# Optimization experiments

Hardware: AMD Instinct MI355X
Metric: run time of the kernel (lower is better)

The kernel has to match this reference:

```python
import jax, jax.numpy as jnp
import numpy as np

D_MODEL = 1024
N_HEADS = 16
HEAD_DIM = D_MODEL // N_HEADS
D_LATENT = 256
LAMBDA_DECAY = 0.01
TIME_STEP = 0.01  # get_timestamps spacing; wall-clock base cancels in diffs
CLAMP = 1e4


def setup_inputs() -> dict:
    key = jax.random.key(0)
    ks = jax.random.split(key, 8)
    B, S = 2, 2048
    def w(k, i, o):
        return jax.random.normal(k, (i, o), dtype=jnp.float32) * 0.02
    return {
        "x": jax.random.normal(ks[0], (B, S, D_MODEL), dtype=jnp.float32),
        "Wq": w(ks[1], D_MODEL, D_MODEL),
        "Wk": w(ks[2], D_MODEL, D_MODEL),
        "Wv": w(ks[3], D_MODEL, D_MODEL),
        "Wo": w(ks[4], D_MODEL, D_MODEL),
        "W_down_kv": w(ks[5], D_MODEL, D_LATENT),
        "W_up_k": w(ks[6], D_LATENT, D_MODEL),
        "W_up_v": w(ks[7], D_LATENT, D_MODEL),
    }


def reference(x, Wq, Wk, Wv, Wo, W_down_kv, W_up_k, W_up_v):
    B, S, _ = x.shape
    q = x @ Wq
    k = x @ Wk
    v = x @ Wv
    latent_kv = (k + v) @ W_down_kv            # [B,S,d_latent]
    k_rec = latent_kv @ W_up_k                 # [B,S,d_model]
    v_rec = latent_kv @ W_up_v
    # split heads -> [B,H,S,hd]
    def heads(t):
        return t.reshape(B, S, N_HEADS, HEAD_DIM).transpose(0, 2, 1, 3)
    qh, kh, vh = heads(q), heads(k_rec), heads(v_rec)
    scale = 1.0 / (jnp.sqrt(jnp.float32(D_MODEL)) + 1e-8)
    scores = jnp.einsum("bhqd,bhkd->bhqk", qh, kh) * scale
    scores = jnp.clip(jnp.nan_to_num(scores, nan=-1e9), -CLAMP, CLAMP)
    # time decay: |t_i - t_j| = TIME_STEP * |i - j| (wall-clock base cancels)
    idx = jnp.arange(S, dtype=jnp.float32)
    decay = jnp.exp(-LAMBDA_DECAY * TIME_STEP * jnp.abs(idx[:, None] - idx[None, :]))
    scores = scores * decay[None, None, :, :]
    scores = jnp.clip(jnp.nan_to_num(scores, nan=-1e9), -CLAMP, CLAMP)
    attn = jax.nn.softmax(scores, axis=-1)
    out = jnp.einsum("bhqk,bhkd->bhqd", attn, vh)
    out = out.transpose(0, 2, 1, 3).reshape(B, S, D_MODEL)
    return out @ Wo, latent_kv
```

## Files before the change

kernel.cpp:

```cpp
#include <hip/hip_runtime.h>
#include <hip/hip_bf16.h>
#include <cstdint>
#include <cstddef>

typedef __bf16 bf16;
typedef __bf16 bf16x8 __attribute__((ext_vector_type(8)));
typedef float f32x4 __attribute__((ext_vector_type(4)));

#define NB 2
#define SEQ 2048
#define DM 1024
#define MTOK 4096
#define DL 256
#define NH 16
#define HD 64

#define LOG2E 1.4426950408889634f

__device__ __forceinline__ void gload16(const void* g, void* l) {
  __builtin_amdgcn_global_load_lds((const __attribute__((address_space(1))) void*)g,
                                   (__attribute__((address_space(3))) void*)l, 16, 0, 0);
}
__device__ __forceinline__ float fast_exp2(float x) {
#if __has_builtin(__builtin_amdgcn_exp2f)
  return __builtin_amdgcn_exp2f(x);
#else
  float r; asm("v_exp_f32 %0, %1" : "=v"(r) : "v"(x)); return r;
#endif
}
__device__ __forceinline__ int xcd_swz(int orig, int nwg) {
  int x = orig & 7;
  int q = nwg >> 3, r = nwg & 7;
  int base = (x < r) ? x * (q + 1) : r * (q + 1) + (x - r) * q;
  return base + (orig >> 3);
}

__device__ __forceinline__ void transpose_dev(const float* __restrict__ in0,
                                              bf16* __restrict__ out, int R, int C,
                                              int c0, int r0, int tid, float (*tile)[33]) {
  int tx = tid & 31, ty = tid >> 5;
#pragma unroll
  for (int i = 0; i < 4; ++i) {
    int r = r0 + ty + 8 * i;
    tile[ty + 8 * i][tx] = in0[(size_t)r * C + c0 + tx];
  }
  __syncthreads();
  int c = tid >> 3, s = tid & 7;
  bf16 o4[4] __attribute__((aligned(8)));
#pragma unroll
  for (int j = 0; j < 4; ++j) o4[j] = (bf16)tile[4 * s + j][c];
  *reinterpret_cast<uint2*>(out + (size_t)(c0 + c) * R + r0 + 4 * s) =
      *reinterpret_cast<const uint2*>(o4);
}

__device__ __forceinline__ void cvt8_dev(const float* __restrict__ in, bf16* __restrict__ out,
                                         int blk, int tid) {
  int i = (blk * 256 + tid) * 8;
  float4 a = *reinterpret_cast<const float4*>(in + i);
  float4 b = *reinterpret_cast<const float4*>(in + i + 4);
  bf16 o[8] __attribute__((aligned(16)));
  o[0] = (bf16)a.x; o[1] = (bf16)a.y; o[2] = (bf16)a.z; o[3] = (bf16)a.w;
  o[4] = (bf16)b.x; o[5] = (bf16)b.y; o[6] = (bf16)b.z; o[7] = (bf16)b.w;
  *reinterpret_cast<uint4*>(out + i) = *reinterpret_cast<const uint4*>(o);
}

__device__ __forceinline__ void sum8_dev(const float* __restrict__ in0, const float* __restrict__ in1,
                                         bf16* __restrict__ out, int blk, int tid) {
  int i = (blk * 256 + tid) * 8;
  float4 a0 = *reinterpret_cast<const float4*>(in0 + i);
  float4 b0 = *reinterpret_cast<const float4*>(in0 + i + 4);
  float4 a1 = *reinterpret_cast<const float4*>(in1 + i);
  float4 b1 = *reinterpret_cast<const float4*>(in1 + i + 4);
  bf16 o[8] __attribute__((aligned(16)));
  o[0] = (bf16)(a0.x + a1.x); o[1] = (bf16)(a0.y + a1.y);
  o[2] = (bf16)(a0.z + a1.z); o[3] = (bf16)(a0.w + a1.w);
  o[4] = (bf16)(b0.x + b1.x); o[5] = (bf16)(b0.y + b1.y);
  o[6] = (bf16)(b0.z + b1.z); o[7] = (bf16)(b0.w + b1.w);
  *reinterpret_cast<uint4*>(out + i) = *reinterpret_cast<const uint4*>(o);
}

__global__ __launch_bounds__(256) void prep_kernel(const float* __restrict__ x,
                                                   const float* __restrict__ Wq,
                                                   const float* __restrict__ Wk,
                                                   const float* __restrict__ Wv,
                                                   const float* __restrict__ Wo,
                                                   const float* __restrict__ Wdn,
                                                   const float* __restrict__ Wuk,
                                                   const float* __restrict__ Wuv,
                                                   bf16* xbf, bf16* WqT, bf16* WoT, bf16* WdnT,
                                                   bf16* WukT, bf16* WuvT, bf16* Wkv) {
  __shared__ float tile[32][33];
  int id = blockIdx.x, tid = threadIdx.x;
  if (id < 2048) { cvt8_dev(x, xbf, id, tid); return; }
  id -= 2048;
  if (id < 512) { sum8_dev(Wk, Wv, Wkv, id, tid); return; }
  id -= 512;
  if (id < 1024) { transpose_dev(Wq, WqT, 1024, 1024, (id & 31) * 32, (id >> 5) * 32, tid, tile); return; }
  id -= 1024;
  if (id < 1024) { transpose_dev(Wo, WoT, 1024, 1024, (id & 31) * 32, (id >> 5) * 32, tid, tile); return; }
  id -= 1024;
  if (id < 256) { transpose_dev(Wdn, WdnT, 1024, 256, (id & 7) * 32, (id >> 3) * 32, tid, tile); return; }
  id -= 256;
  if (id < 256) { transpose_dev(Wuk, WukT, 256, 1024, (id & 31) * 32, (id >> 5) * 32, tid, tile); return; }
  id -= 256;
  transpose_dev(Wuv, WuvT, 256, 1024, (id & 31) * 32, (id >> 5) * 32, tid, tile);
}

template <int TN, int EPI>
__device__ __forceinline__ void gemm_core(const bf16* __restrict__ A, const bf16* __restrict__ Bt,
                                          bf16* __restrict__ O1, bf16* __restrict__ O2,
                                          float* __restrict__ Of,
                                          int K, int bx, int by, bf16* As, bf16* Bs) {
  const int tid = threadIdx.x;
  const int lane = tid & 63;
  const int wv = tid >> 6;
  const int wr = wv >> 1, wc = wv & 1;
  const int row0 = bx * 128, col0 = by * TN;
  const int l15 = lane & 15;
  const int kq = (lane >> 4) * 8;
  constexpr int NR = TN / 32;
  constexpr int BSZ = TN * 32;

  const bf16* aS = A + (size_t)(row0 + (tid >> 2)) * K + (tid & 3) * 8;
  const bf16* bS = Bt + (size_t)(col0 + (tid >> 2)) * K + (tid & 3) * 8;
  const int d0 = tid * 8, d1 = tid * 8 + 2048;

  gload16(aS, As + d0); gload16(aS + (size_t)64 * K, As + d1);
  gload16(bS, Bs + d0);
  if constexpr (TN == 128) gload16(bS + (size_t)64 * K, Bs + d1);
  aS += 32; bS += 32;

  f32x4 acc[4][NR] = {};
  int cur = 0;
  for (int k0 = 0; k0 < K; k0 += 32) {
    __syncthreads();
    if (k0 + 32 < K) {
      const int nxA = (cur ^ 1) * 4096, nxB = (cur ^ 1) * BSZ;
      gload16(aS, As + nxA + d0); gload16(aS + (size_t)64 * K, As + nxA + d1);
      gload16(bS, Bs + nxB + d0);
      if constexpr (TN == 128) gload16(bS + (size_t)64 * K, Bs + nxB + d1);
      aS += 32; bS += 32;
    }
    const bf16* Ab = As + cur * 4096;
    const bf16* Bb = Bs + cur * BSZ;
    bf16x8 af[4], bfr[NR];
#pragma unroll
    for (int m = 0; m < 4; ++m)
      af[m] = *reinterpret_cast<const bf16x8*>(&Ab[(wr * 64 + m * 16 + l15) * 32 + kq]);
#pragma unroll
    for (int n = 0; n < NR; ++n)
      bfr[n] = *reinterpret_cast<const bf16x8*>(&Bb[(wc * (TN / 2) + n * 16 + l15) * 32 + kq]);
    __builtin_amdgcn_s_setprio(1);
#pragma unroll
    for (int m = 0; m < 4; ++m)
#pragma unroll
      for (int n = 0; n < NR; ++n)
        acc[m][n] = __builtin_amdgcn_mfma_f32_16x16x32_bf16(af[m], bfr[n], acc[m][n], 0, 0, 0);
    __builtin_amdgcn_s_setprio(0);
    cur ^= 1;
  }

  const int rbase = row0 + wr * 64 + (lane >> 4) * 4;
  const int cbase = col0 + wc * (TN / 2) + l15;
#pragma unroll
  for (int m = 0; m < 4; ++m) {
#pragma unroll
    for (int n = 0; n < NR; ++n) {
      const int cc = cbase + n * 16;
      if constexpr (EPI == 0) {
#pragma unroll
        for (int r = 0; r < 4; ++r)
          O1[(size_t)(rbase + m * 16 + r) * DM + cc] = (bf16)acc[m][n][r];
      } else if constexpr (EPI == 3) {
#pragma unroll
        for (int r = 0; r < 4; ++r)
          Of[(size_t)(rbase + m * 16 + r) * DM + cc] = acc[m][n][r];
      } else if constexpr (EPI == 6) {
#pragma unroll
        for (int r = 0; r < 4; ++r) {
          float v = acc[m][n][r];
          O1[(size_t)(rbase + m * 16 + r) * DL + cc] = (bf16)v;
          Of[(size_t)(rbase + m * 16 + r) * DL + cc] = v;
        }
      } else {
#pragma unroll
        for (int r = 0; r < 4; ++r)
          O1[(size_t)(rbase + m * 16 + r) * MTOK + cc] = (bf16)acc[m][n][r];
      }
    }
  }
}

__global__ __launch_bounds__(256) void gemm_q_w(const bf16* __restrict__ xbf,
                                                const bf16* __restrict__ WqT, bf16* qbf,
                                                const bf16* __restrict__ WdnT,
                                                const bf16* __restrict__ Wkv, bf16* WkvdT) {
  __shared__ __align__(16) bf16 As[2 * 4096];
  __shared__ __align__(16) bf16 Bs[2 * 64 * 32];
  int id = xcd_swz(blockIdx.x, 544);
  if (id < 32)
    gemm_core<64, 0>(WdnT, Wkv, WkvdT, nullptr, nullptr, DM, id >> 4, id & 15, As, Bs);
  else {
    int j = id - 32;
    gemm_core<64, 0>(xbf, WqT, qbf, nullptr, nullptr, DM, j >> 4, j & 15, As, Bs);
  }
}

__global__ __launch_bounds__(256) void gemm_latent(const bf16* __restrict__ xbf,
                                                   const bf16* __restrict__ WkvdT,
                                                   bf16* latbf, float* out_lat) {
  __shared__ __align__(16) bf16 As[2 * 4096];
  __shared__ __align__(16) bf16 Bs[2 * 64 * 32];
  int id = xcd_swz(blockIdx.x, 128);
  gemm_core<64, 6>(xbf, WkvdT, latbf, nullptr, out_lat, DM, id >> 2, id & 3, As, Bs);
}

__global__ __launch_bounds__(256) void gemm_up(const bf16* __restrict__ latbf,
                                               const bf16* __restrict__ WukT,
                                               const bf16* __restrict__ WuvT,
                                               bf16* kbuf, bf16* vT) {
  __shared__ __align__(16) bf16 As[2 * 4096];
  __shared__ __align__(16) bf16 Bs[2 * 64 * 32];
  int id = xcd_swz(blockIdx.x, 1024);
  if (id < 512)
    gemm_core<64, 0>(latbf, WukT, kbuf, nullptr, nullptr, DL, id >> 4, id & 15, As, Bs);
  else {
    int j = id - 512;
    gemm_core<64, 7>(WuvT, latbf, vT, nullptr, nullptr, DL, j >> 6, j & 63, As, Bs);
  }
}

__global__ __launch_bounds__(256) void gemm_out(const bf16* __restrict__ ctx,
                                                const bf16* __restrict__ WoT, float* out0) {
  __shared__ __align__(16) bf16 As[2 * 4096];
  __shared__ __align__(16) bf16 Bs[2 * 64 * 32];
  int id = xcd_swz(blockIdx.x, 512);
  gemm_core<64, 3>(ctx, WoT, nullptr, nullptr, out0, DM, id >> 4, id & 15, As, Bs);
}

__global__ __launch_bounds__(256) void attn_kernel(const bf16* __restrict__ Q,
                                                   const bf16* __restrict__ Kr,
                                                   const bf16* __restrict__ Vt,
                                                   bf16* __restrict__ Ctx) {
  __shared__ __align__(16) bf16 Ks[2 * 4096];
  __shared__ __align__(16) bf16 Vs[2 * 4096];
  __shared__ __align__(16) bf16 Ps[4096];
  const int work = xcd_swz(blockIdx.x, SEQ / 64 * NH * NB);
  const int qt = work & 31, h = (work >> 5) & 15, b = work >> 9;
  const int tid = threadIdx.x, lane = tid & 63, wv = tid >> 6;
  const int l15 = lane & 15, lg = lane >> 4;
  const int qbase = qt * 64 + wv * 16;
  const size_t tok0 = (size_t)b * SEQ;

  bf16x8 qf[2];
  {
    const bf16* qp = Q + (tok0 + qbase + l15) * DM + h * HD + lg * 8;
    qf[0] = *reinterpret_cast<const bf16x8*>(qp);
    qf[1] = *reinterpret_cast<const bf16x8*>(qp + 32);
  }

  const int c1 = tid + 256;
  const int r0s = tid >> 3, r1s = c1 >> 3;
  const int cc0 = (tid & 7) ^ (r0s & 7), cc1 = (c1 & 7) ^ (r1s & 7);
  const bf16* kS0 = Kr + (tok0 + r0s) * DM + h * HD + cc0 * 8;
  const bf16* kS1 = Kr + (tok0 + r1s) * DM + h * HD + cc1 * 8;
  const bf16* vS0 = Vt + (size_t)(h * HD + r0s) * MTOK + tok0 + cc0 * 8;
  const bf16* vS1 = Vt + (size_t)(h * HD + r1s) * MTOK + tok0 + cc1 * 8;
  const int d0 = tid * 8, d1 = tid * 8 + 2048;

  gload16(kS0, Ks + d0); gload16(kS1, Ks + d1);
  gload16(vS0, Vs + d0); gload16(vS1, Vs + d1);
  kS0 += 64 * DM; kS1 += 64 * DM; vS0 += 64; vS1 += 64;

  int koff[2][4], poffw[4], poffr[2];
  const int hsw = l15 & 7;
#pragma unroll
  for (int ks = 0; ks < 2; ++ks)
#pragma unroll
    for (int nf = 0; nf < 4; ++nf) {
      int row = nf * 16 + l15;
      koff[ks][nf] = row * 64 + (((ks * 4 + lg) ^ (row & 7)) * 8);
    }
  const int psBase = wv * 1024 + l15 * 64;
#pragma unroll
  for (int nf = 0; nf < 4; ++nf)
    poffw[nf] = psBase + (((nf * 2 + (lg >> 1)) ^ hsw) * 8) + (lg & 1) * 4;
#pragma unroll
  for (int ks = 0; ks < 2; ++ks)
    poffr[ks] = psBase + (((ks * 4 + lg) ^ hsw) * 8);

  bf16x8 ones;
#pragma unroll
  for (int j = 0; j < 8; ++j) ones[j] = (bf16)1.0f;

  f32x4 oacc[4] = {};
  f32x4 lacc = {};
  float dec[4][4];
  const float DEC2C = (1.0f / 32.0f) * LOG2E;
  const float NC2 = -1.0e-4f * LOG2E;
  const float E64 = 0.99362048f, IE64 = 1.00642051f;
  const int ib = -qbase - l15 + lg * 4;

  int cur = 0;
  for (int t = 0; t < SEQ / 64; ++t) {
    const int key0 = t * 64;
    __syncthreads();
    if (t + 1 < SEQ / 64) {
      const int nx = (cur ^ 1) * 4096;
      gload16(kS0, Ks + nx + d0); gload16(kS1, Ks + nx + d1);
      gload16(vS0, Vs + nx + d0); gload16(vS1, Vs + nx + d1);
      kS0 += 64 * DM; kS1 += 64 * DM; vS0 += 64; vS1 += 64;
    }
    {
      bool before = (key0 + 63 < qbase);
      bool afterp = (key0 >= qbase + 79);
      if (t == 0 || (!before && !afterp)) {
#pragma unroll
        for (int nf = 0; nf < 4; ++nf)
#pragma unroll
          for (int r = 0; r < 4; ++r) {
            float df = (float)(key0 + ib + nf * 16 + r);
            dec[nf][r] = DEC2C * fast_exp2(NC2 * fabsf(df));
          }
      } else {
        float mlt = before ? IE64 : E64;
#pragma unroll
        for (int nf = 0; nf < 4; ++nf)
#pragma unroll
          for (int r = 0; r < 4; ++r) dec[nf][r] *= mlt;
      }
    }
    const int kb = cur * 4096;

    f32x4 sc[4] = {};
    __builtin_amdgcn_s_setprio(1);
#pragma unroll
    for (int ks = 0; ks < 2; ++ks)
#pragma unroll
      for (int nf = 0; nf < 4; ++nf) {
        bf16x8 kf = *reinterpret_cast<const bf16x8*>(&Ks[kb + koff[ks][nf]]);
        sc[nf] = __builtin_amdgcn_mfma_f32_16x16x32_bf16(kf, qf[ks], sc[nf], 0, 0, 0);
      }
    __builtin_amdgcn_s_setprio(0);

#pragma unroll
    for (int nf = 0; nf < 4; ++nf) {
      bf16 t4[4] __attribute__((aligned(8)));
#pragma unroll
      for (int r = 0; r < 4; ++r) t4[r] = (bf16)fast_exp2(sc[nf][r] * dec[nf][r]);
      *reinterpret_cast<uint2*>(&Ps[poffw[nf]]) = *reinterpret_cast<const uint2*>(t4);
    }
    bf16x8 pb[2];
    pb[0] = *reinterpret_cast<const bf16x8*>(&Ps[poffr[0]]);
    pb[1] = *reinterpret_cast<const bf16x8*>(&Ps[poffr[1]]);

    __builtin_amdgcn_s_setprio(1);
#pragma unroll
    for (int ks = 0; ks < 2; ++ks) {
#pragma unroll
      for (int nf = 0; nf < 4; ++nf) {
        bf16x8 vf = *reinterpret_cast<const bf16x8*>(&Vs[kb + koff[ks][nf]]);
        oacc[nf] = __builtin_amdgcn_mfma_f32_16x16x32_bf16(vf, pb[ks], oacc[nf], 0, 0, 0);
      }
      lacc = __builtin_amdgcn_mfma_f32_16x16x32_bf16(ones, pb[ks], lacc, 0, 0, 0);
    }
    __builtin_amdgcn_s_setprio(0);
    cur ^= 1;
  }

  const float inv = 1.0f / lacc[0];
#pragma unroll
  for (int nf = 0; nf < 4; ++nf) {
    bf16 o4[4] __attribute__((aligned(8)));
#pragma unroll
    for (int r = 0; r < 4; ++r) o4[r] = (bf16)(oacc[nf][r] * inv);
    *reinterpret_cast<uint2*>(Ctx + (tok0 + qbase + l15) * DM + h * HD + nf * 16 + lg * 4) =
        *reinterpret_cast<const uint2*>(o4);
  }
}

extern "C" void kernel_launch(void* const* d_in, const int* in_sizes, int n_in,
                              void* d_out, int out_size, void* d_ws, size_t ws_size,
                              hipStream_t stream) {
  const float* x   = (const float*)d_in[0];
  const float* Wq  = (const float*)d_in[1];
  const float* Wk  = (const float*)d_in[2];
  const float* Wv  = (const float*)d_in[3];
  const float* Wo  = (const float*)d_in[4];
  const float* Wdn = (const float*)d_in[5];
  const float* Wuk = (const float*)d_in[6];
  const float* Wuv = (const float*)d_in[7];
  float* out0 = (float*)d_out;
  float* out_lat = out0 + (size_t)MTOK * DM;

  char* ws = (char*)d_ws;
  const size_t MB = 1u << 20;
  bf16* xbf   = (bf16*)(ws + 0);
  bf16* qbf   = (bf16*)(ws + 8 * MB);
  bf16* kbuf  = (bf16*)(ws + 16 * MB);
  bf16* Wkv   = kbuf;
  bf16* WkvdT = (bf16*)(ws + 18 * MB);
  bf16* vT    = (bf16*)(ws + 24 * MB);
  bf16* latbf = (bf16*)(ws + 32 * MB);
  bf16* WqT   = (bf16*)(ws + 34 * MB);
  bf16* WoT   = (bf16*)(ws + 36 * MB);
  bf16* WukT  = (bf16*)(ws + 38 * MB);
  bf16* WuvT  = (bf16*)(ws + 38 * MB + 512 * 1024);
  bf16* WdnT  = (bf16*)(ws + 39 * MB);
  bf16* ctx   = xbf;

  prep_kernel<<<5376, 256, 0, stream>>>(x, Wq, Wk, Wv, Wo, Wdn, Wuk, Wuv,
                                        xbf, WqT, WoT, WdnT, WukT, WuvT, Wkv);
  gemm_q_w<<<544, 256, 0, stream>>>(xbf, WqT, qbf, WdnT, Wkv, WkvdT);
  gemm_latent<<<128, 256, 0, stream>>>(xbf, WkvdT, latbf, out_lat);
  gemm_up<<<1024, 256, 0, stream>>>(latbf, WukT, WuvT, kbuf, vT);
  attn_kernel<<<1024, 256, 0, stream>>>(qbf, kbuf, vT, ctx);
  gemm_out<<<512, 256, 0, stream>>>(ctx, WoT, out0);

  (void)in_sizes; (void)n_in; (void)out_size; (void)ws_size;
}
```

Baseline: 134.9 us.

## Share K/V tiles across 128-query attention blocks and retile latent GEMM to 64x64

The attention kernel now runs 8 waves per block, each covering 128 query rows. Every K/V tile loaded into shared memory is therefore reused by twice as many queries, and each thread issues one async load per tile instead of two. The latent projection GEMM moves to a dedicated 64x64-tile routine with 256 blocks instead of 128, to fill more compute units. The trade-off is larger blocks with more shared memory (doubled P buffer), fewer attention blocks in flight, and a smaller per-wave MFMA tile in the latent GEMM.

```diff
diff --git a/kernel.cpp b/kernel.cpp
--- a/kernel.cpp
+++ b/kernel.cpp
@@ -108,8 +108,7 @@
 
 template <int TN, int EPI>
 __device__ __forceinline__ void gemm_core(const bf16* __restrict__ A, const bf16* __restrict__ Bt,
-                                          bf16* __restrict__ O1, bf16* __restrict__ O2,
-                                          float* __restrict__ Of,
+                                          bf16* __restrict__ O1, float* __restrict__ Of,
                                           int K, int bx, int by, bf16* As, bf16* Bs) {
   const int tid = threadIdx.x;
   const int lane = tid & 63;
@@ -175,13 +174,6 @@
 #pragma unroll
         for (int r = 0; r < 4; ++r)
           Of[(size_t)(rbase + m * 16 + r) * DM + cc] = acc[m][n][r];
-      } else if constexpr (EPI == 6) {
-#pragma unroll
-        for (int r = 0; r < 4; ++r) {
-          float v = acc[m][n][r];
-          O1[(size_t)(rbase + m * 16 + r) * DL + cc] = (bf16)v;
-          Of[(size_t)(rbase + m * 16 + r) * DL + cc] = v;
-        }
       } else {
 #pragma unroll
         for (int r = 0; r < 4; ++r)
@@ -189,6 +181,66 @@
       }
     }
   }
+}
+
+__device__ __forceinline__ void gemm64_lat(const bf16* __restrict__ A, const bf16* __restrict__ Bt,
+                                           bf16* __restrict__ O1, float* __restrict__ Of,
+                                           int K, int bx, int by, bf16* As, bf16* Bs) {
+  const int tid = threadIdx.x;
+  const int lane = tid & 63;
+  const int wv = tid >> 6;
+  const int wr = wv >> 1, wc = wv & 1;
+  const int row0 = bx * 64, col0 = by * 64;
+  const int l15 = lane & 15;
+  const int kq = (lane >> 4) * 8;
+
+  const bf16* aS = A + (size_t)(row0 + (tid >> 2)) * K + (tid & 3) * 8;
+  const bf16* bS = Bt + (size_t)(col0 + (tid >> 2)) * K + (tid & 3) * 8;
+  const int d0 = tid * 8;
+
+  gload16(aS, As + d0); gload16(bS, Bs + d0);
+  aS += 32; bS += 32;
+
+  f32x4 acc[2][2] = {};
+  int cur = 0;
+  for (int k0 = 0; k0 < K; k0 += 32) {
+    __syncthreads();
+    if (k0 + 32 < K) {
+      const int nx = (cur ^ 1) * 2048;
+      gload16(aS, As + nx + d0); gload16(bS, Bs + nx + d0);
+      aS += 32; bS += 32;
+    }
+    const bf16* Ab = As + cur * 2048;
+    const bf16* Bb = Bs + cur * 2048;
+    bf16x8 af[2], bfr[2];
+#pragma unroll
+    for (int m = 0; m < 2; ++m)
+      af[m] = *reinterpret_cast<const bf16x8*>(&Ab[(wr * 32 + m * 16 + l15) * 32 + kq]);
+#pragma unroll
+    for (int n = 0; n < 2; ++n)
+      bfr[n] = *reinterpret_cast<const bf16x8*>(&Bb[(wc * 32 + n * 16 + l15) * 32 + kq]);
+    __builtin_amdgcn_s_setprio(1);
+#pragma unroll
+    for (int m = 0; m < 2; ++m)
+#pragma unroll
+      for (int n = 0; n < 2; ++n)
+        acc[m][n] = __builtin_amdgcn_mfma_f32_16x16x32_bf16(af[m], bfr[n], acc[m][n], 0, 0, 0);
+    __builtin_amdgcn_s_setprio(0);
+    cur ^= 1;
+  }
+
+  const int rbase = row0 + wr * 32 + (lane >> 4) * 4;
+  const int cbase = col0 + wc * 32 + l15;
+#pragma unroll
+  for (int m = 0; m < 2; ++m)
+#pragma unroll
+    for (int n = 0; n < 2; ++n)
+#pragma unroll
+      for (int r = 0; r < 4; ++r) {
+        float v = acc[m][n][r];
+        O1[(size_t)(rbase + m * 16 + r) * DL + (cbase + n * 16)] = (bf16)v;
+        Of[(size_t)(rbase + m * 16 + r) * DL + (cbase + n * 16)] = v;
+      }
 }
 
 __global__ __launch_bounds__(256) void gemm_q_w(const bf16* __restrict__ xbf,
@@ -199,20 +251,20 @@
   __shared__ __align__(16) bf16 Bs[2 * 64 * 32];
   int id = xcd_swz(blockIdx.x, 544);
   if (id < 32)
-    gemm_core<64, 0>(WdnT, Wkv, WkvdT, nullptr, nullptr, DM, id >> 4, id & 15, As, Bs);
+    gemm_core<64, 0>(WdnT, Wkv, WkvdT, nullptr, DM, id >> 4, id & 15, As, Bs);
   else {
     int j = id - 32;
-    gemm_core<64, 0>(xbf, WqT, qbf, nullptr, nullptr, DM, j >> 4, j & 15, As, Bs);
+    gemm_core<64, 0>(xbf, WqT, qbf, nullptr, DM, j >> 4, j & 15, As, Bs);
   }
 }
 
 __global__ __launch_bounds__(256) void gemm_latent(const bf16* __restrict__ xbf,
                                                    const bf16* __restrict__ WkvdT,
                                                    bf16* latbf, float* out_lat) {
-  __shared__ __align__(16) bf16 As[2 * 4096];
-  __shared__ __align__(16) bf16 Bs[2 * 64 * 32];
-  int id = xcd_swz(blockIdx.x, 128);
-  gemm_core<64, 6>(xbf, WkvdT, latbf, nullptr, out_lat, DM, id >> 2, id & 3, As, Bs);
+  __shared__ __align__(16) bf16 As[2 * 2048];
+  __shared__ __align__(16) bf16 Bs[2 * 2048];
+  int id = xcd_swz(blockIdx.x, 256);
+  gemm64_lat(xbf, WkvdT, latbf, out_lat, DM, id >> 2, id & 3, As, Bs);
 }
 
 __global__ __launch_bounds__(256) void gemm_up(const bf16* __restrict__ latbf,
@@ -223,10 +275,10 @@
   __shared__ __align__(16) bf16 Bs[2 * 64 * 32];
   int id = xcd_swz(blockIdx.x, 1024);
   if (id < 512)
-    gemm_core<64, 0>(latbf, WukT, kbuf, nullptr, nullptr, DL, id >> 4, id & 15, As, Bs);
+    gemm_core<64, 0>(latbf, WukT, kbuf, nullptr, DL, id >> 4, id & 15, As, Bs);
   else {
     int j = id - 512;
-    gemm_core<64, 7>(WuvT, latbf, vT, nullptr, nullptr, DL, j >> 6, j & 63, As, Bs);
+    gemm_core<64, 7>(WuvT, latbf, vT, nullptr, DL, j >> 6, j & 63, As, Bs);
   }
 }
 
@@ -235,21 +287,21 @@
   __shared__ __align__(16) bf16 As[2 * 4096];
   __shared__ __align__(16) bf16 Bs[2 * 64 * 32];
   int id = xcd_swz(blockIdx.x, 512);
-  gemm_core<64, 3>(ctx, WoT, nullptr, nullptr, out0, DM, id >> 4, id & 15, As, Bs);
-}
-
-__global__ __launch_bounds__(256) void attn_kernel(const bf16* __restrict__ Q,
+  gemm_core<64, 3>(ctx, WoT, nullptr, out0, DM, id >> 4, id & 15, As, Bs);
+}
+
+__global__ __launch_bounds__(512) void attn_kernel(const bf16* __restrict__ Q,
                                                    const bf16* __restrict__ Kr,
                                                    const bf16* __restrict__ Vt,
                                                    bf16* __restrict__ Ctx) {
   __shared__ __align__(16) bf16 Ks[2 * 4096];
   __shared__ __align__(16) bf16 Vs[2 * 4096];
-  __shared__ __align__(16) bf16 Ps[4096];
-  const int work = xcd_swz(blockIdx.x, SEQ / 64 * NH * NB);
-  const int qt = work & 31, h = (work >> 5) & 15, b = work >> 9;
+  __shared__ __align__(16) bf16 Ps[8192];
+  const int work = xcd_swz(blockIdx.x, SEQ / 128 * NH * NB);
+  const int qt = work & 15, h = (work >> 4) & 15, b = work >> 8;
   const int tid = threadIdx.x, lane = tid & 63, wv = tid >> 6;
   const int l15 = lane & 15, lg = lane >> 4;
-  const int qbase = qt * 64 + wv * 16;
+  const int qbase = qt * 128 + wv * 16;
   const size_t tok0 = (size_t)b * SEQ;
 
   bf16x8 qf[2];
@@ -259,18 +311,15 @@
     qf[1] = *reinterpret_cast<const bf16x8*>(qp + 32);
   }
 
-  const int c1 = tid + 256;
-  const int r0s = tid >> 3, r1s = c1 >> 3;
-  const int cc0 = (tid & 7) ^ (r0s & 7), cc1 = (c1 & 7) ^ (r1s & 7);
+  const int r0s = tid >> 3;
+  const int cc0 = (tid & 7) ^ (r0s & 7);
   const bf16* kS0 = Kr + (tok0 + r0s) * DM + h * HD + cc0 * 8;
-  const bf16* kS1 = Kr + (tok0 + r1s) * DM + h * HD + cc1 * 8;
   const bf16* vS0 = Vt + (size_t)(h * HD + r0s) * MTOK + tok0 + cc0 * 8;
-  const bf16* vS1 = Vt + (size_t)(h * HD + r1s) * MTOK + tok0 + cc1 * 8;
-  const int d0 = tid * 8, d1 = tid * 8 + 2048;
-
-  gload16(kS0, Ks + d0); gload16(kS1, Ks + d1);
-  gload16(vS0, Vs + d0); gload16(vS1, Vs + d1);
-  kS0 += 64 * DM; kS1 += 64 * DM; vS0 += 64; vS1 += 64;
+  const int d0 = tid * 8;
+
+  gload16(kS0, Ks + d0);
+  gload16(vS0, Vs + d0);
+  kS0 += 64 * DM; vS0 += 64;
 
   int koff[2][4], poffw[4], poffr[2];
   const int hsw = l15 & 7;
@@ -307,9 +356,9 @@
     __syncthreads();
     if (t + 1 < SEQ / 64) {
       const int nx = (cur ^ 1) * 4096;
-      gload16(kS0, Ks + nx + d0); gload16(kS1, Ks + nx + d1);
-      gload16(vS0, Vs + nx + d0); gload16(vS1, Vs + nx + d1);
-      kS0 += 64 * DM; kS1 += 64 * DM; vS0 += 64; vS1 += 64;
+      gload16(kS0, Ks + nx + d0);
+      gload16(vS0, Vs + nx + d0);
+      kS0 += 64 * DM; vS0 += 64;
     }
     {
       bool before = (key0 + 63 < qbase);
@@ -412,9 +461,9 @@
   prep_kernel<<<5376, 256, 0, stream>>>(x, Wq, Wk, Wv, Wo, Wdn, Wuk, Wuv,
                                         xbf, WqT, WoT, WdnT, WukT, WuvT, Wkv);
   gemm_q_w<<<544, 256, 0, stream>>>(xbf, WqT, qbf, WdnT, Wkv, WkvdT);
-  gemm_latent<<<128, 256, 0, stream>>>(xbf, WkvdT, latbf, out_lat);
+  gemm_latent<<<256, 256, 0, stream>>>(xbf, WkvdT, latbf, out_lat);
   gemm_up<<<1024, 256, 0, stream>>>(latbf, WukT, WuvT, kbuf, vT);
-  attn_kernel<<<1024, 256, 0, stream>>>(qbf, kbuf, vT, ctx);
+  attn_kernel<<<512, 512, 0, stream>>>(qbf, kbuf, vT, ctx);
   gemm_out<<<512, 256, 0, stream>>>(ctx, WoT, out0);
 
   (void)in_sizes; (void)n_in; (void)out_size; (void)ws_size;
```

After: 123.2 us. -8.6%, faster.
